# Kernel tuning notes

Measured on AMD Instinct MI355X. Metric: run time of the kernel, lower is better.

## Reference

```python
import jax, jax.numpy as jnp
import numpy as np

B, S, D = 2, 2048, 1024
H = 16
DH = D // H
FFN = 4096
EPS = 1e-5
SCALE = 1.0 / np.sqrt(DH).astype(np.float32)


def layer_norm(x, g, b):
    mu = jnp.mean(x, axis=-1, keepdims=True)
    var = jnp.mean(jnp.square(x - mu), axis=-1, keepdims=True)
    return (x - mu) * jax.lax.rsqrt(var + EPS) * g + b


def setup_inputs() -> dict:
    key = jax.random.key(0)
    ks = jax.random.split(key, 12)
    std = 0.02
    return {
        "x": jax.random.normal(ks[0], (B, S, D), dtype=jnp.float32),
        "mask": jax.random.randint(ks[1], (B, S), 0, 2, dtype=jnp.int32),
        "w_qkv": jax.random.normal(ks[2], (D, 3 * D), dtype=jnp.float32) * std,
        "w_out": jax.random.normal(ks[3], (D, D), dtype=jnp.float32) * std,
        "b_out": jnp.zeros((D,), dtype=jnp.float32),
        "g1": jnp.ones((D,), dtype=jnp.float32),
        "be1": jnp.zeros((D,), dtype=jnp.float32),
        "g2": jnp.ones((D,), dtype=jnp.float32),
        "be2": jnp.zeros((D,), dtype=jnp.float32),
        "w1": jax.random.normal(ks[4], (D, FFN), dtype=jnp.float32) * std,
        "b1": jnp.zeros((FFN,), dtype=jnp.float32),
        "w2": jax.random.normal(ks[5], (FFN, D), dtype=jnp.float32) * std,
        "b2": jnp.zeros((D,), dtype=jnp.float32),
    }


def reference(x, mask, w_qkv, w_out, b_out, g1, be1, g2, be2, w1, b1, w2, b2):
    # --- pre-norm self-attention ---
    h = layer_norm(x, g1, be1)                              # [B,S,D]
    qkv = (h @ w_qkv).reshape(B, S, 3, H, DH)               # [B,S,3,H,Dh]
    q, k, v = [jnp.transpose(qkv[:, :, i], (0, 2, 1, 3)) for i in range(3)]  # [B,H,S,Dh]
    scores = jnp.einsum("bhqd,bhkd->bhqk", q, k) * SCALE    # [B,H,S,S]
    key_mask = (mask != 0)[:, None, None, :]                # [B,1,1,S]
    scores = jnp.where(key_mask, scores, -1e9)
    attn = jax.nn.softmax(scores, axis=-1)
    out = jnp.einsum("bhqk,bhkd->bhqd", attn, v)            # [B,H,S,Dh]
    out = jnp.transpose(out, (0, 2, 1, 3)).reshape(B, S, D)
    x = x + (out @ w_out + b_out)
    # --- pre-norm FFN ---
    h2 = layer_norm(x, g2, be2)
    ffn = jax.nn.relu(h2 @ w1 + b1) @ w2 + b2
    return x + ffn
```

## Files before the change

### kernel.cpp

```cpp
#include <hip/hip_runtime.h>

typedef unsigned short u16;
typedef __bf16 bf16x8 __attribute__((ext_vector_type(8)));
typedef float f32x4 __attribute__((ext_vector_type(4)));

typedef __attribute__((address_space(1))) const void* as1cv;
typedef __attribute__((address_space(3))) void* as3v;

__device__ __forceinline__ u16 f2bf(float f) {
  union { float f; unsigned u; } v;
  v.f = f;
  unsigned r = (v.u + 0x7fffu + ((v.u >> 16) & 1u)) >> 16;
  return (u16)r;
}

__device__ __forceinline__ unsigned cvtpk(float lo, float hi) {
  unsigned r;
  asm("v_cvt_pk_bf16_f32 %0, %1, %2" : "=v"(r) : "v"(lo), "v"(hi));
  return r;
}

__device__ __forceinline__ void gload16(const void* g, void* l) {
  __builtin_amdgcn_global_load_lds((as1cv)g, (as3v)l, 16, 0, 0);
}

__global__ __launch_bounds__(256)
void ln_kernel(const float* __restrict__ x, const float* __restrict__ g,
               const float* __restrict__ be, u16* __restrict__ out) {
  __shared__ float red[8];
  const int row = blockIdx.x;
  const int tid = threadIdx.x;
  const float4 v = ((const float4*)(x + (size_t)row * 1024))[tid];
  float s = v.x + v.y + v.z + v.w;
#pragma unroll
  for (int off = 1; off < 64; off <<= 1) s += __shfl_xor(s, off, 64);
  const int wv = tid >> 6, lane = tid & 63;
  if (lane == 0) red[wv] = s;
  __syncthreads();
  s = red[0] + red[1] + red[2] + red[3];
  const float mu = s * (1.0f / 1024.0f);
  const float d0 = v.x - mu, d1 = v.y - mu, d2 = v.z - mu, d3 = v.w - mu;
  float q = d0 * d0 + d1 * d1 + d2 * d2 + d3 * d3;
#pragma unroll
  for (int off = 1; off < 64; off <<= 1) q += __shfl_xor(q, off, 64);
  if (lane == 0) red[4 + wv] = q;
  __syncthreads();
  q = red[4] + red[5] + red[6] + red[7];
  const float inv = rsqrtf(q * (1.0f / 1024.0f) + 1e-5f);
  const float4 gv = ((const float4*)g)[tid];
  const float4 bv = ((const float4*)be)[tid];
  unsigned p0 = (unsigned)f2bf(d0 * inv * gv.x + bv.x) |
                ((unsigned)f2bf(d1 * inv * gv.y + bv.y) << 16);
  unsigned p1 = (unsigned)f2bf(d2 * inv * gv.z + bv.z) |
                ((unsigned)f2bf(d3 * inv * gv.w + bv.w) << 16);
  uint2 o; o.x = p0; o.y = p1;
  *(uint2*)(out + (size_t)row * 1024 + tid * 4) = o;
}

__global__ __launch_bounds__(256)
void transpose_all(const float* __restrict__ i0, u16* __restrict__ o0,
                   const float* __restrict__ i1, u16* __restrict__ o1,
                   const float* __restrict__ i2, u16* __restrict__ o2,
                   const float* __restrict__ i3, u16* __restrict__ o3) {
  __shared__ float t[32][33];
  int id = blockIdx.x;
  const float* in; u16* out; int K, N, nx;
  if (id < 3072)      { in = i0; out = o0; K = 1024; N = 3072; nx = 96; }
  else if (id < 4096) { id -= 3072; in = i1; out = o1; K = 1024; N = 1024; nx = 32; }
  else if (id < 8192) { id -= 4096; in = i2; out = o2; K = 1024; N = 4096; nx = 128; }
  else                { id -= 8192; in = i3; out = o3; K = 4096; N = 1024; nx = 32; }
  const int n0 = (id % nx) * 32, k0 = (id / nx) * 32;
  const int tx = threadIdx.x & 31, ty = threadIdx.x >> 5;
  for (int r = ty; r < 32; r += 8)
    t[r][tx] = in[(size_t)(k0 + r) * N + n0 + tx];
  __syncthreads();
  for (int r = ty; r < 32; r += 8)
    out[(size_t)(n0 + r) * K + k0 + tx] = f2bf(t[tx][r]);
}

template<int BIAS, int RELU, int RES, int MODE, int NSPLIT>
__global__ __launch_bounds__(256, 2)
void gemm_bt(const u16* __restrict__ A, const u16* __restrict__ Bt,
             const float* __restrict__ bias, const float* __restrict__ res,
             void* __restrict__ C, u16* __restrict__ vt,
             int M, int N, int K, int kChunk) {
  __shared__ u16 As[4][4096];
  __shared__ u16 Bs[4][4096];
  const int tid = threadIdx.x;
  const int wv = tid >> 6, lane = tid & 63;
  const int z = (NSPLIT > 1) ? (int)(blockIdx.x % NSPLIT) : 0;
  const int bm = (int)(blockIdx.x / NSPLIT) * 128;
  const int bn = blockIdx.y * 128;
  const int wr = wv >> 1, wc = wv & 1;
  const int l16 = lane & 15, lh = lane >> 4;

  const int ssk = ((lane & 3) ^ ((lane >> 3) & 3)) << 3;
  const int rdk = (lh ^ ((l16 >> 1) & 3)) << 3;

  f32x4 acc[4][4] = {};

  const int kb = z * kChunk;
  const u16* Ag = A + (size_t)(bm + wv * 16 + (lane >> 2)) * K + kb + ssk;
  const u16* Bg = Bt + (size_t)(bn + wv * 16 + (lane >> 2)) * K + kb + ssk;

#define STG_A(buf, ko)  do { \
    gload16(Ag + (ko), &As[buf][wv * 512]); \
    gload16(Ag + (size_t)64 * K + (ko), &As[buf][2048 + wv * 512]); } while (0)
#define STG_B(buf, ko)  do { \
    gload16(Bg + (ko), &Bs[buf][wv * 512]); \
    gload16(Bg + (size_t)64 * K + (ko), &Bs[buf][2048 + wv * 512]); } while (0)

  const int nst = kChunk >> 5;
  STG_A(0, 0); STG_B(0, 0);
  if (nst > 1) { STG_A(1, 32); STG_B(1, 32); }
  if (nst > 2) { STG_A(2, 64); STG_B(2, 64); }

  for (int t = 0; t < nst; ++t) {
    const int cur = t & 3;
    const int rem = nst - t;
    if (rem >= 3)      asm volatile("s_waitcnt vmcnt(8)" ::: "memory");
    else if (rem == 2) asm volatile("s_waitcnt vmcnt(4)" ::: "memory");
    else               asm volatile("s_waitcnt vmcnt(0)" ::: "memory");
    __builtin_amdgcn_s_barrier();
    asm volatile("" ::: "memory");
    const int nxb = (t + 3) & 3;
    bf16x8 af[4], bfv[4];
#pragma unroll
    for (int i = 0; i < 4; i++)
      af[i] = *(const bf16x8*)&As[cur][(wr * 64 + i * 16 + l16) * 32 + rdk];
#pragma unroll
    for (int j = 0; j < 2; j++)
      bfv[j] = *(const bf16x8*)&Bs[cur][(wc * 64 + j * 16 + l16) * 32 + rdk];
    if (t + 3 < nst) STG_A(nxb, (t + 3) * 32);
    __builtin_amdgcn_s_setprio(1);
#pragma unroll
    for (int i = 0; i < 4; i++)
#pragma unroll
      for (int j = 0; j < 2; j++)
        acc[i][j] = __builtin_amdgcn_mfma_f32_16x16x32_bf16(af[i], bfv[j], acc[i][j], 0, 0, 0);
    __builtin_amdgcn_s_setprio(0);
#pragma unroll
    for (int j = 2; j < 4; j++)
      bfv[j] = *(const bf16x8*)&Bs[cur][(wc * 64 + j * 16 + l16) * 32 + rdk];
    if (t + 3 < nst) STG_B(nxb, (t + 3) * 32);
    __builtin_amdgcn_s_setprio(1);
#pragma unroll
    for (int i = 0; i < 4; i++)
#pragma unroll
      for (int j = 2; j < 4; j++)
        acc[i][j] = __builtin_amdgcn_mfma_f32_16x16x32_bf16(af[i], bfv[j], acc[i][j], 0, 0, 0);
    __builtin_amdgcn_s_setprio(0);
  }
#undef STG_A
#undef STG_B

#pragma unroll
  for (int i = 0; i < 4; i++) {
#pragma unroll
    for (int j = 0; j < 4; j++) {
      const int col = bn + wc * 64 + j * 16 + l16;
      const float bv = (BIAS && z == 0) ? bias[col] : 0.0f;
      if (MODE == 3 && bn >= 2048) {
        const int cc = col - 2048, h = cc >> 6, d = cc & 63;
        const int row0 = bm + wr * 64 + i * 16 + (lane >> 4) * 4;
        const int bb = row0 >> 11, kv0 = row0 & 2047;
        const int p0 = (kv0 & 32) | (((kv0 >> 2) & 3) << 3) | (((kv0 >> 4) & 1) << 2);
        uint2 o;
        o.x = (unsigned)f2bf(acc[i][j][0]) | ((unsigned)f2bf(acc[i][j][1]) << 16);
        o.y = (unsigned)f2bf(acc[i][j][2]) | ((unsigned)f2bf(acc[i][j][3]) << 16);
        *(uint2*)(vt + ((size_t)(bb * 16 + h) * 64 + d) * 2048 + (kv0 & ~63) + p0) = o;
      } else {
#pragma unroll
        for (int r = 0; r < 4; r++) {
          const int row = bm + wr * 64 + i * 16 + (lane >> 4) * 4 + r;
          float v = acc[i][j][r] + bv;
          if (RELU) v = fmaxf(v, 0.0f);
          if (RES) v += res[(size_t)row * N + col];
          if (MODE == 2)       atomicAdd((float*)C + (size_t)row * N + col, v);
          else if (MODE == 0)  ((float*)C)[(size_t)row * N + col] = v;
          else                 ((u16*)C)[(size_t)row * N + col] = f2bf(v);
        }
      }
    }
  }
}

__global__ __launch_bounds__(256, 4)
void attn3(const u16* __restrict__ qkv, const u16* __restrict__ vT,
           const int* __restrict__ mask, u16* __restrict__ aout) {
  __shared__ u16 KsS[2][4096];
  __shared__ u16 VsS[2][4096];
  __shared__ float mbL[2048];

  const int tid = threadIdx.x;
  const int wv = tid >> 6, lane = tid & 63;
  const int l16 = lane & 15, lh = lane >> 4;
  const int bh = blockIdx.x, b = bh >> 4, h = bh & 15;
  const int q0 = blockIdx.y * 64 + wv * 16;

  {
    const int4* srcm = (const int4*)(mask + b * 2048);
    float4* dstm = (float4*)mbL;
#pragma unroll
    for (int u = 0; u < 2; ++u) {
      const int4 mv = srcm[tid + u * 256];
      float4 f;
      f.x = mv.x ? 0.f : -1.4426950408889634e9f;
      f.y = mv.y ? 0.f : -1.4426950408889634e9f;
      f.z = mv.z ? 0.f : -1.4426950408889634e9f;
      f.w = mv.w ? 0.f : -1.4426950408889634e9f;
      dstm[tid + u * 256] = f;
    }
  }

  bf16x8 qf[2];
#pragma unroll
  for (int c = 0; c < 2; ++c)
    qf[c] = *(const bf16x8*)(qkv + (size_t)(b * 2048 + q0 + l16) * 3072 + h * 64 + c * 32 + 8 * lh);

  const int rs = (l16 & 7) << 4;
  const int koff0 = ((16 * lh) ^ rs) >> 1;
  const int koff1 = ((64 + 16 * lh) ^ rs) >> 1;
  const int voff0 = koff0, voff1 = koff1;

  const int rl0 = wv * 8 + (lane >> 3);
  const int rl1 = 32 + wv * 8 + (lane >> 3);
  const int glog = (lane & 7) ^ ((lane >> 3) & 7);
  const u16* kg0 = qkv + (size_t)(b * 2048 + rl0) * 3072 + 1024 + h * 64 + 8 * glog;
  const u16* kg1 = qkv + (size_t)(b * 2048 + rl1) * 3072 + 1024 + h * 64 + 8 * glog;
  const u16* vg0 = vT + ((size_t)bh * 64 + rl0) * 2048 + 8 * glog;
  const u16* vg1 = vT + ((size_t)bh * 64 + rl1) * 2048 + 8 * glog;

  gload16(kg0, &KsS[0][wv * 512]);
  gload16(kg1, &KsS[0][2048 + wv * 512]);
  gload16(vg0, &VsS[0][wv * 512]);
  gload16(vg1, &VsS[0][2048 + wv * 512]);
  kg0 += 64 * 3072; kg1 += 64 * 3072; vg0 += 64; vg1 += 64;

  const float CL2 = 0.125f * 1.4426950408889634f;
  float lacc = 0.f;
  f32x4 oT[4] = {};

  for (int t = 0; t < 32; ++t) {
    asm volatile("s_waitcnt vmcnt(0)" ::: "memory");
    __syncthreads();
    const int cur = t & 1;
    if (t + 1 < 32) {
      const int nx = cur ^ 1;
      gload16(kg0, &KsS[nx][wv * 512]);
      gload16(kg1, &KsS[nx][2048 + wv * 512]);
      gload16(vg0, &VsS[nx][wv * 512]);
      gload16(vg1, &VsS[nx][2048 + wv * 512]);
      kg0 += 64 * 3072; kg1 += 64 * 3072; vg0 += 64; vg1 += 64;
    }

    const u16* Kb = &KsS[cur][0];
    const u16* Vb = &VsS[cur][0];

    f32x4 mbc[4];
#pragma unroll
    for (int n = 0; n < 4; ++n)
      mbc[n] = *(const f32x4*)&mbL[t * 64 + n * 16 + 4 * lh];

    f32x4 s[4] = {};
    __builtin_amdgcn_s_setprio(1);
#pragma unroll
    for (int c = 0; c < 2; ++c) {
      const int ko = c ? koff1 : koff0;
      bf16x8 kf[4];
#pragma unroll
      for (int n = 0; n < 4; ++n)
        kf[n] = *(const bf16x8*)(Kb + (n * 16 + l16) * 64 + ko);
#pragma unroll
      for (int n = 0; n < 4; ++n)
        s[n] = __builtin_amdgcn_mfma_f32_16x16x32_bf16(kf[n], qf[c], s[n], 0, 0, 0);
    }
    __builtin_amdgcn_s_setprio(0);

#pragma unroll
    for (int n = 0; n < 4; ++n)
#pragma unroll
      for (int j = 0; j < 4; ++j) {
        const float p = __builtin_exp2f(fmaf(s[n][j], CL2, mbc[n][j]));
        s[n][j] = p;
        lacc += p;
      }

    union U8 { unsigned u[4]; bf16x8 v; };
    U8 pa[2];
#pragma unroll
    for (int u = 0; u < 2; ++u) {
      pa[u].u[0] = cvtpk(s[2 * u][0], s[2 * u][1]);
      pa[u].u[1] = cvtpk(s[2 * u][2], s[2 * u][3]);
      pa[u].u[2] = cvtpk(s[2 * u + 1][0], s[2 * u + 1][1]);
      pa[u].u[3] = cvtpk(s[2 * u + 1][2], s[2 * u + 1][3]);
    }

    __builtin_amdgcn_s_setprio(1);
#pragma unroll
    for (int u = 0; u < 2; ++u) {
      const int vo = u ? voff1 : voff0;
#pragma unroll
      for (int D = 0; D < 4; ++D) {
        const bf16x8 va = *(const bf16x8*)(Vb + (D * 16 + l16) * 64 + vo);
        oT[D] = __builtin_amdgcn_mfma_f32_16x16x32_bf16(va, pa[u].v, oT[D], 0, 0, 0);
      }
    }
    __builtin_amdgcn_s_setprio(0);
  }

  lacc += __shfl_xor(lacc, 16, 64);
  lacc += __shfl_xor(lacc, 32, 64);
  const float rr = 1.0f / lacc;
#pragma unroll
  for (int D = 0; D < 4; ++D) {
    uint2 o;
    o.x = cvtpk(oT[D][0] * rr, oT[D][1] * rr);
    o.y = cvtpk(oT[D][2] * rr, oT[D][3] * rr);
    *(uint2*)(aout + (size_t)(b * 2048 + q0 + l16) * 1024 + h * 64 + D * 16 + 4 * lh) = o;
  }
}

extern "C" void kernel_launch(void* const* d_in, const int* in_sizes, int n_in,
                              void* d_out, int out_size, void* d_ws, size_t ws_size,
                              hipStream_t stream) {
  (void)in_sizes; (void)n_in; (void)out_size; (void)ws_size;
  const float* x     = (const float*)d_in[0];
  const int*   mask  = (const int*)d_in[1];
  const float* w_qkv = (const float*)d_in[2];
  const float* w_out = (const float*)d_in[3];
  const float* b_out = (const float*)d_in[4];
  const float* g1    = (const float*)d_in[5];
  const float* be1   = (const float*)d_in[6];
  const float* g2    = (const float*)d_in[7];
  const float* be2   = (const float*)d_in[8];
  const float* w1    = (const float*)d_in[9];
  const float* b1    = (const float*)d_in[10];
  const float* w2    = (const float*)d_in[11];
  const float* b2    = (const float*)d_in[12];
  float* out = (float*)d_out;

  char* ws = (char*)d_ws;
  u16* hA    = (u16*)(ws);
  u16* wqkvT = (u16*)(ws + 8388608);
  u16* woutT = (u16*)(ws + 14680064);
  u16* w1T   = (u16*)(ws + 16777216);
  u16* w2T   = (u16*)(ws + 25165824);
  u16* qkv   = (u16*)(ws + 33554432);
  u16* ffn1  = (u16*)(ws + 33554432);
  u16* vTb   = (u16*)(ws + 67108864);
  u16* aout  = (u16*)(ws + 75497472);

  ln_kernel<<<4096, 256, 0, stream>>>(x, g1, be1, hA);
  transpose_all<<<12288, 256, 0, stream>>>(w_qkv, wqkvT, w_out, woutT, w1, w1T, w2, w2T);
  gemm_bt<0, 0, 0, 3, 1><<<dim3(32, 24), 256, 0, stream>>>(hA, wqkvT, nullptr, nullptr, qkv, vTb, 4096, 3072, 1024, 1024);
  attn3<<<dim3(32, 32), 256, 0, stream>>>(qkv, vTb, mask, aout);
  gemm_bt<1, 0, 1, 0, 1><<<dim3(32, 8), 256, 0, stream>>>(aout, woutT, b_out, x, out, nullptr, 4096, 1024, 1024, 1024);
  ln_kernel<<<4096, 256, 0, stream>>>(out, g2, be2, hA);
  gemm_bt<1, 1, 0, 1, 1><<<dim3(32, 32), 256, 0, stream>>>(hA, w1T, b1, nullptr, ffn1, nullptr, 4096, 4096, 1024, 1024);
  gemm_bt<1, 0, 0, 2, 2><<<dim3(64, 8), 256, 0, stream>>>(ffn1, w2T, b2, nullptr, out, nullptr, 4096, 1024, 4096, 2048);
}
```

Before: 257.3 us.

## Add 256x256-tile 512-thread GEMM for QKV and FFN1 projections

```diff
diff --git a/kernel.cpp b/kernel.cpp
--- a/kernel.cpp
+++ b/kernel.cpp
@@ -185,6 +185,99 @@
   }
 }
 
+template<int BIAS, int RELU, int MODE>
+__global__ __launch_bounds__(512, 2)
+void gemm256(const u16* __restrict__ A, const u16* __restrict__ Bt,
+             const float* __restrict__ bias, u16* __restrict__ C,
+             u16* __restrict__ vt, int M, int N, int K) {
+  __shared__ u16 As[2][16384];
+  __shared__ u16 Bs[2][16384];
+  const int tid = threadIdx.x;
+  const int wv = tid >> 6, lane = tid & 63;
+  const int l16 = lane & 15, lh = lane >> 4;
+  const int wm = wv >> 2, wn = wv & 3;
+  const int bm = blockIdx.x * 256, bn = blockIdx.y * 256;
+
+  const int koff = ((lane & 7) ^ ((lane >> 3) & 7)) << 3;
+  const int ka0 = ((lh ^ (l16 & 7)) << 3);
+  const int ka1 = (((4 + lh) ^ (l16 & 7)) << 3);
+
+  f32x4 acc[8][4] = {};
+
+  const u16* Ag = A + (size_t)(bm + wv * 8 + (lane >> 3)) * K + koff;
+  const u16* Bg = Bt + (size_t)(bn + wv * 8 + (lane >> 3)) * K + koff;
+
+#define STAGE256(buf, ko)                                                  \
+  do {                                                                     \
+    _Pragma("unroll")                                                      \
+    for (int j = 0; j < 4; ++j) {                                          \
+      gload16(Ag + (size_t)(j * 64) * K + (ko), &As[buf][j * 4096 + wv * 512]); \
+      gload16(Bg + (size_t)(j * 64) * K + (ko), &Bs[buf][j * 4096 + wv * 512]); \
+    }                                                                      \
+  } while (0)
+
+  const int nt = K >> 6;
+  STAGE256(0, 0);
+  if (nt > 1) STAGE256(1, 64);
+
+  for (int t = 0; t < nt; ++t) {
+    const int cur = t & 1;
+    if (t + 1 < nt) asm volatile("s_waitcnt vmcnt(8)" ::: "memory");
+    else            asm volatile("s_waitcnt vmcnt(0)" ::: "memory");
+    __builtin_amdgcn_s_barrier();
+    asm volatile("" ::: "memory");
+#pragma unroll
+    for (int kk = 0; kk < 2; ++kk) {
+      const int ko = kk ? ka1 : ka0;
+      bf16x8 af[8], bfv[4];
+#pragma unroll
+      for (int i = 0; i < 8; ++i)
+        af[i] = *(const bf16x8*)&As[cur][(wm * 128 + i * 16 + l16) * 64 + ko];
+#pragma unroll
+      for (int n = 0; n < 4; ++n)
+        bfv[n] = *(const bf16x8*)&Bs[cur][(wn * 64 + n * 16 + l16) * 64 + ko];
+      __builtin_amdgcn_s_setprio(1);
+#pragma unroll
+      for (int i = 0; i < 8; ++i)
+#pragma unroll
+        for (int n = 0; n < 4; ++n)
+          acc[i][n] = __builtin_amdgcn_mfma_f32_16x16x32_bf16(af[i], bfv[n], acc[i][n], 0, 0, 0);
+      __builtin_amdgcn_s_setprio(0);
+    }
+    asm volatile("" ::: "memory");
+    __builtin_amdgcn_s_barrier();
+    asm volatile("" ::: "memory");
+    if (t + 2 < nt) STAGE256(cur, (t + 2) * 64);
+  }
+#undef STAGE256
+
+#pragma unroll
+  for (int i = 0; i < 8; ++i)
+#pragma unroll
+    for (int n = 0; n < 4; ++n) {
+      const int col = bn + wn * 64 + n * 16 + l16;
+      const float bv = BIAS ? bias[col] : 0.0f;
+      if (MODE == 3 && bn >= 2048) {
+        const int cc = col - 2048, h = cc >> 6, d = cc & 63;
+        const int row0 = bm + wm * 128 + i * 16 + lh * 4;
+        const int bb = row0 >> 11, kv0 = row0 & 2047;
+        const int p0 = (kv0 & 32) | (((kv0 >> 2) & 3) << 3) | (((kv0 >> 4) & 1) << 2);
+        uint2 o;
+        o.x = (unsigned)f2bf(acc[i][n][0]) | ((unsigned)f2bf(acc[i][n][1]) << 16);
+        o.y = (unsigned)f2bf(acc[i][n][2]) | ((unsigned)f2bf(acc[i][n][3]) << 16);
+        *(uint2*)(vt + ((size_t)(bb * 16 + h) * 64 + d) * 2048 + (kv0 & ~63) + p0) = o;
+      } else {
+#pragma unroll
+        for (int r = 0; r < 4; ++r) {
+          const int row = bm + wm * 128 + i * 16 + lh * 4 + r;
+          float v = acc[i][n][r] + bv;
+          if (RELU) v = fmaxf(v, 0.0f);
+          C[(size_t)row * N + col] = f2bf(v);
+        }
+      }
+    }
+}
+
 __global__ __launch_bounds__(256, 4)
 void attn3(const u16* __restrict__ qkv, const u16* __restrict__ vT,
            const int* __restrict__ mask, u16* __restrict__ aout) {
@@ -353,10 +446,10 @@
 
   ln_kernel<<<4096, 256, 0, stream>>>(x, g1, be1, hA);
   transpose_all<<<12288, 256, 0, stream>>>(w_qkv, wqkvT, w_out, woutT, w1, w1T, w2, w2T);
-  gemm_bt<0, 0, 0, 3, 1><<<dim3(32, 24), 256, 0, stream>>>(hA, wqkvT, nullptr, nullptr, qkv, vTb, 4096, 3072, 1024, 1024);
+  gemm256<0, 0, 3><<<dim3(16, 12), 512, 0, stream>>>(hA, wqkvT, nullptr, qkv, vTb, 4096, 3072, 1024);
   attn3<<<dim3(32, 32), 256, 0, stream>>>(qkv, vTb, mask, aout);
   gemm_bt<1, 0, 1, 0, 1><<<dim3(32, 8), 256, 0, stream>>>(aout, woutT, b_out, x, out, nullptr, 4096, 1024, 1024, 1024);
   ln_kernel<<<4096, 256, 0, stream>>>(out, g2, be2, hA);
-  gemm_bt<1, 1, 0, 1, 1><<<dim3(32, 32), 256, 0, stream>>>(hA, w1T, b1, nullptr, ffn1, nullptr, 4096, 4096, 1024, 1024);
+  gemm256<1, 1, 1><<<dim3(16, 16), 512, 0, stream>>>(hA, w1T, b1, ffn1, nullptr, 4096, 4096, 1024);
   gemm_bt<1, 0, 0, 2, 2><<<dim3(64, 8), 256, 0, stream>>>(ffn1, w2T, b2, nullptr, out, nullptr, 4096, 1024, 4096, 2048);
 }
```

Result: faster. 251.1 us (-2.4%).
